# Optimization experiments

Measured on AMD Instinct MI355X. Metric: run time of the kernel, lower is better.

Reference implementation:

```python
import jax, jax.numpy as jnp
import numpy as np

NUM_NODES = 2048
NUM_REL = 8
HIDDEN = 256


def setup_inputs() -> dict:
    key = jax.random.key(0)
    k1, k2, k3 = jax.random.split(key, 3)
    X = jax.random.normal(k1, (NUM_NODES, HIDDEN, NUM_REL), dtype=jnp.float32)
    A = jax.random.uniform(k2, (NUM_NODES, NUM_NODES, NUM_REL), dtype=jnp.float32)
    # nn.init.normal_(std=0.01)
    weight = 0.01 * jax.random.normal(k3, (HIDDEN, HIDDEN, NUM_REL), dtype=jnp.float32)
    return {"X": X, "A": A, "weight": weight}


def _tensor_product(A, B):
    # Faithful to the original: FFT along last (relation) dim, take REAL part of
    # both transformed operands, per-slice matmul, then real part of ifft.
    Af = jnp.real(jnp.fft.fft(A, axis=-1))  # (n1, n2, k)
    Bf = jnp.real(jnp.fft.fft(B, axis=-1))  # (n2, n4, k)
    C = jnp.einsum('nmk,mhk->nhk', Af, Bf)  # batched real matmul over slices k
    return jnp.real(jnp.fft.ifft(C, axis=-1)).astype(A.dtype)


def reference(X, A, weight):
    res = _tensor_product(A, X)          # (num_nodes, hidden, num_rel)
    res = _tensor_product(res, weight)   # (num_nodes, hidden, num_rel)
    return res
```

## Files before the change

kernel.cpp:

```cpp
#include <hip/hip_runtime.h>


typedef __bf16 bf16_t;
typedef __bf16 bf16x2 __attribute__((ext_vector_type(2)));
typedef __bf16 bf16x8 __attribute__((ext_vector_type(8)));
typedef float f32x4 __attribute__((ext_vector_type(4)));

#define R2C 0.70710678118654752f

__device__ __forceinline__ size_t swz(int r, int c, int K) {
  return (size_t)r * K + (c & ~63) + ((((c >> 3) & 7) ^ (r & 7)) << 3) + (c & 7);
}

__device__ __forceinline__ void async_cp16(const void* g, void* l) {
  __builtin_amdgcn_global_load_lds((const __attribute__((address_space(1))) char*)g,
                                   (__attribute__((address_space(3))) char*)l,
                                   16, 0, 0);
}

__device__ __forceinline__ void fwd5(const float x[8], float F[5]) {
  float s04 = x[0] + x[4], d04 = x[0] - x[4];
  float s26 = x[2] + x[6];
  float s15 = x[1] + x[5], s37 = x[3] + x[7];
  float t = (x[1] + x[7]) - (x[3] + x[5]);
  float e = s04 + s26, o = s15 + s37;
  F[0] = e + o;
  F[1] = d04 + R2C * t;
  F[2] = s04 - s26;
  F[3] = d04 - R2C * t;
  F[4] = e - o;
}

__global__ __launch_bounds__(256) void k_pre(const float* __restrict__ X,
                                             const float* __restrict__ A,
                                             const float* __restrict__ W,
                                             bf16_t* __restrict__ Xft,
                                             bf16_t* __restrict__ Af,
                                             bf16_t* __restrict__ Wft) {
  int b = blockIdx.x;
  if (b < 8192) {
    size_t t = (size_t)b * 256 + threadIdx.x;
    size_t idx = t * 2;
    int n = (int)(idx >> 11), m = (int)(idx & 2047);
    const float4* p = (const float4*)(A + idx * 8);
    float4 q0 = p[0], q1 = p[1], q2 = p[2], q3 = p[3];
    float x0[8] = {q0.x, q0.y, q0.z, q0.w, q1.x, q1.y, q1.z, q1.w};
    float x1[8] = {q2.x, q2.y, q2.z, q2.w, q3.x, q3.y, q3.z, q3.w};
    float F0[5], F1[5];
    fwd5(x0, F0);
    fwd5(x1, F1);
    size_t pos = swz(n, m, 2048);
#pragma unroll
    for (int j = 0; j < 5; j++) {
      bf16x2 v = {(bf16_t)F0[j], (bf16_t)F1[j]};
      *(bf16x2*)(Af + (size_t)j * 4194304 + pos) = v;
    }
  } else if (b < 9216) {
    size_t t = (size_t)(b - 8192) * 256 + threadIdx.x;
    size_t p0 = t * 2;
#pragma unroll
    for (int u = 0; u < 2; u++) {
      size_t pp = p0 + u;
      int m = (int)(pp >> 8), h = (int)(pp & 255);
      const float4* p = (const float4*)(X + pp * 8);
      float4 a = p[0], bb = p[1];
      float x[8] = {a.x, a.y, a.z, a.w, bb.x, bb.y, bb.z, bb.w};
      float F[5];
      fwd5(x, F);
      size_t pos = swz(h, m, 2048);
#pragma unroll
      for (int j = 0; j < 5; j++)
        Xft[(size_t)j * 524288 + pos] = (bf16_t)F[j];
    }
  } else {
    int h = b - 9216;
    int hp = threadIdx.x;
    const float4* p = (const float4*)(W + ((size_t)hp * 256 + h) * 8);
    float4 a = p[0], bb = p[1];
    float x[8] = {a.x, a.y, a.z, a.w, bb.x, bb.y, bb.z, bb.w};
    float F[5];
    fwd5(x, F);
    const float sc[5] = {0.125f, 0.25f, 0.25f, 0.25f, 0.125f};
    size_t pos = swz(h, hp, 256);
#pragma unroll
    for (int j = 0; j < 5; j++)
      Wft[(size_t)j * 65536 + pos] = (bf16_t)(F[j] * sc[j]);
  }
}

template <typename OutT, bool SWZ_OUT>
__global__ __launch_bounds__(256) void gemm_lds(const bf16_t* __restrict__ A,
                                                const bf16_t* __restrict__ B,
                                                OutT* __restrict__ C, int K,
                                                size_t ap, size_t bp, size_t cp) {
  __shared__ bf16_t As[128 * 64];
  __shared__ bf16_t Bs[128 * 64];
  const int j = blockIdx.z;
  const bf16_t* Aj = A + (size_t)j * ap;
  const bf16_t* Bj = B + (size_t)j * bp;
  OutT* Cj = C + (size_t)j * cp;
  const int n0 = blockIdx.x * 128, h0 = blockIdx.y * 128;
  const int tid = threadIdx.x;
  const int wv = tid >> 6, ln = tid & 63;
  const int quad = ln >> 4, l16 = ln & 15;
  const int wn = (wv & 1) * 64, wh = (wv >> 1) * 64;

  const bf16_t* ga[4];
  const bf16_t* gb[4];
  bf16_t* la[4];
  bf16_t* lb[4];
#pragma unroll
  for (int s = 0; s < 4; s++) {
    int slot = s * 256 + tid;
    int row = slot >> 3, c16 = slot & 7;
    ga[s] = Aj + (size_t)(n0 + row) * K + c16 * 8;
    gb[s] = Bj + (size_t)(h0 + row) * K + c16 * 8;
    int base = (s * 256 + wv * 64) * 8;
    la[s] = As + base;
    lb[s] = Bs + base;
  }

  f32x4 acc[4][4] = {};
  for (int kk = 0; kk < K; kk += 64) {
    __syncthreads();
#pragma unroll
    for (int s = 0; s < 4; s++) {
      async_cp16(ga[s] + kk, la[s]);
      async_cp16(gb[s] + kk, lb[s]);
    }
    __syncthreads();
#pragma unroll
    for (int kh = 0; kh < 2; kh++) {
      bf16x8 af[4], bfr[4];
      int c16 = kh * 4 + quad;
#pragma unroll
      for (int i = 0; i < 4; i++) {
        int ra = wn + i * 16 + l16;
        int rb = wh + i * 16 + l16;
        af[i] = *(const bf16x8*)(As + ra * 64 + ((c16 ^ (ra & 7)) << 3));
        bfr[i] = *(const bf16x8*)(Bs + rb * 64 + ((c16 ^ (rb & 7)) << 3));
      }
#pragma unroll
      for (int i = 0; i < 4; i++)
#pragma unroll
        for (int t = 0; t < 4; t++)
          acc[i][t] = __builtin_amdgcn_mfma_f32_16x16x32_bf16(af[i], bfr[t],
                                                              acc[i][t], 0, 0, 0);
    }
  }
#pragma unroll
  for (int i = 0; i < 4; i++) {
#pragma unroll
    for (int t = 0; t < 4; t++) {
      int hc = h0 + wh + t * 16 + l16;
#pragma unroll
      for (int rg = 0; rg < 4; rg++) {
        int nr = n0 + wn + i * 16 + quad * 4 + rg;
        size_t off = SWZ_OUT ? swz(nr, hc, 256) : (size_t)nr * 256 + hc;
        Cj[off] = (OutT)acc[i][t][rg];
      }
    }
  }
}

__global__ __launch_bounds__(256) void k_combine(const float* __restrict__ C2,
                                                 float* __restrict__ out) {
  size_t idx = (size_t)blockIdx.x * 256 + threadIdx.x;
  float c0 = C2[idx];
  float c1 = C2[524288 + idx];
  float c2 = C2[2 * 524288 + idx];
  float c3 = C2[3 * 524288 + idx];
  float c4 = C2[4 * 524288 + idx];
  float o0 = c0 + c1 + c2 + c3 + c4;
  float o4 = c0 - c1 + c2 - c3 + c4;
  float o2 = c0 - c2 + c4;
  float rt = R2C * (c1 - c3);
  float o1 = c0 + rt - c4;
  float o3 = c0 - rt - c4;
  float4* op = (float4*)(out + idx * 8);
  op[0] = make_float4(o0, o1, o2, o3);
  op[1] = make_float4(o4, o3, o2, o1);
}

extern "C" void kernel_launch(void* const* d_in, const int* in_sizes, int n_in,
                              void* d_out, int out_size, void* d_ws, size_t ws_size,
                              hipStream_t stream) {
  const float* X = (const float*)d_in[0];
  const float* A = (const float*)d_in[1];
  const float* W = (const float*)d_in[2];
  float* out = (float*)d_out;
  char* ws = (char*)d_ws;

  bf16_t* Af  = (bf16_t*)(ws);
  bf16_t* Xft = (bf16_t*)(ws + 41943040);
  bf16_t* Wft = (bf16_t*)(ws + 47185920);
  bf16_t* C1  = (bf16_t*)(ws + 47841280);
  float*  C2  = (float*) (ws + 53084160);

  k_pre<<<dim3(9472), 256, 0, stream>>>(X, A, W, Xft, Af, Wft);
  gemm_lds<bf16_t, true><<<dim3(16, 2, 5), 256, 0, stream>>>(
      Af, Xft, C1, 2048, (size_t)4194304, (size_t)524288, (size_t)524288);
  gemm_lds<float, false><<<dim3(16, 2, 5), 256, 0, stream>>>(
      C1, Wft, C2, 256, (size_t)524288, (size_t)65536, (size_t)524288);
  k_combine<<<dim3(2048), 256, 0, stream>>>(C2, out);
}
```

Before: 288.4 us.

## Double-buffer GEMM LDS loads and transpose X FFT output through shared memory

The GEMM now double-buffers its LDS tiles: the next K-slice is issued with async global-to-LDS copies before the current one is computed, and explicit vmcnt waits plus barriers replace the two __syncthreads per iteration. This hides global load latency behind the MFMA work, at the cost of twice the LDS per block. Separately, the X forward-FFT path stages its bf16 results in a shared-memory tile and writes them out as 16-byte swizzled stores instead of scattered 2-byte stores, which reduces the X-branch block count. The added 20KB shared array is declared for every k_pre block, including the A and W branches, which may lower occupancy of the dominant A-transform path.

New measurement: 256.1 us. 1.13x faster.

```diff
diff --git a/kernel.cpp b/kernel.cpp
--- a/kernel.cpp
+++ b/kernel.cpp
@@ -37,6 +37,7 @@
                                              bf16_t* __restrict__ Xft,
                                              bf16_t* __restrict__ Af,
                                              bf16_t* __restrict__ Wft) {
+  __shared__ bf16_t tx[40][256];
   int b = blockIdx.x;
   if (b < 8192) {
     size_t t = (size_t)b * 256 + threadIdx.x;
@@ -55,25 +56,33 @@
       bf16x2 v = {(bf16_t)F0[j], (bf16_t)F1[j]};
       *(bf16x2*)(Af + (size_t)j * 4194304 + pos) = v;
     }
-  } else if (b < 9216) {
-    size_t t = (size_t)(b - 8192) * 256 + threadIdx.x;
-    size_t p0 = t * 2;
-#pragma unroll
-    for (int u = 0; u < 2; u++) {
-      size_t pp = p0 + u;
-      int m = (int)(pp >> 8), h = (int)(pp & 255);
-      const float4* p = (const float4*)(X + pp * 8);
-      float4 a = p[0], bb = p[1];
+  } else if (b < 8448) {
+    int bx = b - 8192;
+    int m0 = (bx & 7) * 256, h0 = (bx >> 3) * 8;
+    int t = threadIdx.x;
+    const float4* p = (const float4*)(X + (((size_t)(m0 + t) * 256) + h0) * 8);
+#pragma unroll
+    for (int h = 0; h < 8; h++) {
+      float4 a = p[2 * h], bb = p[2 * h + 1];
       float x[8] = {a.x, a.y, a.z, a.w, bb.x, bb.y, bb.z, bb.w};
       float F[5];
       fwd5(x, F);
-      size_t pos = swz(h, m, 2048);
-#pragma unroll
-      for (int j = 0; j < 5; j++)
-        Xft[(size_t)j * 524288 + pos] = (bf16_t)F[j];
+#pragma unroll
+      for (int j = 0; j < 5; j++) tx[j * 8 + h][t] = (bf16_t)F[j];
+    }
+    __syncthreads();
+#pragma unroll
+    for (int it = 0; it < 5; it++) {
+      int slot = it * 256 + t;
+      int row = slot >> 5, ch = slot & 31;
+      int j = row >> 3, hl = row & 7;
+      int h = h0 + hl;
+      size_t gpos = (size_t)j * 524288 + (size_t)h * 2048 + m0 +
+                    ((ch & ~7) << 3) + (((ch & 7) ^ (h & 7)) << 3);
+      *(uint4*)(Xft + gpos) = *(const uint4*)(&tx[row][ch * 8]);
     }
   } else {
-    int h = b - 9216;
+    int h = b - 8448;
     int hp = threadIdx.x;
     const float4* p = (const float4*)(W + ((size_t)hp * 256 + h) * 8);
     float4 a = p[0], bb = p[1];
@@ -93,8 +102,7 @@
                                                 const bf16_t* __restrict__ B,
                                                 OutT* __restrict__ C, int K,
                                                 size_t ap, size_t bp, size_t cp) {
-  __shared__ bf16_t As[128 * 64];
-  __shared__ bf16_t Bs[128 * 64];
+  __shared__ bf16_t sm[4 * 8192];
   const int j = blockIdx.z;
   const bf16_t* Aj = A + (size_t)j * ap;
   const bf16_t* Bj = B + (size_t)j * bp;
@@ -107,28 +115,38 @@
 
   const bf16_t* ga[4];
   const bf16_t* gb[4];
-  bf16_t* la[4];
-  bf16_t* lb[4];
+  int lo[4];
 #pragma unroll
   for (int s = 0; s < 4; s++) {
     int slot = s * 256 + tid;
     int row = slot >> 3, c16 = slot & 7;
     ga[s] = Aj + (size_t)(n0 + row) * K + c16 * 8;
     gb[s] = Bj + (size_t)(h0 + row) * K + c16 * 8;
-    int base = (s * 256 + wv * 64) * 8;
-    la[s] = As + base;
-    lb[s] = Bs + base;
+    lo[s] = (s * 256 + wv * 64) * 8;
+  }
+
+#pragma unroll
+  for (int s = 0; s < 4; s++) {
+    async_cp16(ga[s], sm + lo[s]);
+    async_cp16(gb[s], sm + 16384 + lo[s]);
   }
 
   f32x4 acc[4][4] = {};
   for (int kk = 0; kk < K; kk += 64) {
-    __syncthreads();
-#pragma unroll
-    for (int s = 0; s < 4; s++) {
-      async_cp16(ga[s] + kk, la[s]);
-      async_cp16(gb[s] + kk, lb[s]);
-    }
-    __syncthreads();
+    int p = (kk >> 6) & 1;
+    if (kk + 64 < K) {
+#pragma unroll
+      for (int s = 0; s < 4; s++) {
+        async_cp16(ga[s] + kk + 64, sm + (p ^ 1) * 8192 + lo[s]);
+        async_cp16(gb[s] + kk + 64, sm + 16384 + (p ^ 1) * 8192 + lo[s]);
+      }
+      __builtin_amdgcn_s_waitcnt(0xF78);
+    } else {
+      __builtin_amdgcn_s_waitcnt(0xF70);
+    }
+    __builtin_amdgcn_s_barrier();
+    const bf16_t* Asp = sm + p * 8192;
+    const bf16_t* Bsp = sm + 16384 + p * 8192;
 #pragma unroll
     for (int kh = 0; kh < 2; kh++) {
       bf16x8 af[4], bfr[4];
@@ -137,8 +155,8 @@
       for (int i = 0; i < 4; i++) {
         int ra = wn + i * 16 + l16;
         int rb = wh + i * 16 + l16;
-        af[i] = *(const bf16x8*)(As + ra * 64 + ((c16 ^ (ra & 7)) << 3));
-        bfr[i] = *(const bf16x8*)(Bs + rb * 64 + ((c16 ^ (rb & 7)) << 3));
+        af[i] = *(const bf16x8*)(Asp + ra * 64 + ((c16 ^ (ra & 7)) << 3));
+        bfr[i] = *(const bf16x8*)(Bsp + rb * 64 + ((c16 ^ (rb & 7)) << 3));
       }
 #pragma unroll
       for (int i = 0; i < 4; i++)
@@ -147,6 +165,7 @@
           acc[i][t] = __builtin_amdgcn_mfma_f32_16x16x32_bf16(af[i], bfr[t],
                                                               acc[i][t], 0, 0, 0);
     }
+    __builtin_amdgcn_s_barrier();
   }
 #pragma unroll
   for (int i = 0; i < 4; i++) {
@@ -197,7 +216,7 @@
   bf16_t* C1  = (bf16_t*)(ws + 47841280);
   float*  C2  = (float*) (ws + 53084160);
 
-  k_pre<<<dim3(9472), 256, 0, stream>>>(X, A, W, Xft, Af, Wft);
+  k_pre<<<dim3(8704), 256, 0, stream>>>(X, A, W, Xft, Af, Wft);
   gemm_lds<bf16_t, true><<<dim3(16, 2, 5), 256, 0, stream>>>(
       Af, Xft, C1, 2048, (size_t)4194304, (size_t)524288, (size_t)524288);
   gemm_lds<float, false><<<dim3(16, 2, 5), 256, 0, stream>>>(
```
